# Performance work log

Measured on AMD Instinct MI355X. Metric: run time of the kernel, lower is better.

The kernel has to match this reference:

```python
import jax, jax.numpy as jnp
import numpy as np

B, N, D, H, C = 4, 8192, 1024, 16, 128
HD = D // H  # 64
THRESHOLD = 0.99


def setup_inputs() -> dict:
    key = jax.random.key(0)
    ks = jax.random.split(key, 6)
    std = 0.02
    return {
        "x": jax.random.normal(ks[0], (B, N, D), jnp.float32),
        "Wq": jax.random.normal(ks[1], (D, D), jnp.float32) * std,
        "Wk": jax.random.normal(ks[2], (D, D), jnp.float32) * std,
        "Wv": jax.random.normal(ks[3], (D, D), jnp.float32) * std,
        "Wo": jax.random.normal(ks[4], (D, D), jnp.float32) * std,
        "Wf": jax.random.normal(ks[5], (H, D), jnp.float32) * std,
        "delta": jnp.full((H,), float(np.log(THRESHOLD / (1.0 - THRESHOLD))), jnp.float32),
        "norm_weight": jnp.ones((D,), jnp.float32),
    }


def _chunk_scan(qc, kc, vc, lf):
    # qc,kc,vc: [nc, b, H, C, HD]; lf: [nc, b, H, C] inclusive cumsum of log decay within chunk
    mask = jnp.tril(jnp.ones((C, C), bool))
    def step(S, inputs):
        qb, kb, vb, lb = inputs  # [b,H,C,HD], [b,H,C]
        # inter-chunk: q_i decayed by prod of gates up to i, applied to carried state
        o_inter = jnp.einsum('bhid,bhde->bhie', qb * jnp.exp(lb)[..., None], S)
        # intra-chunk: A_ij = (q_i . k_j) * exp(l_i - l_j), j <= i
        A = jnp.einsum('bhid,bhjd->bhij', qb, kb)
        diff = jnp.where(mask, lb[..., :, None] - lb[..., None, :], -jnp.inf)
        A = A * jnp.exp(diff)
        o_intra = jnp.einsum('bhij,bhjd->bhid', A, vb)
        # state update: S <- exp(l_C) * S + sum_j exp(l_C - l_j) k_j v_j^T
        tot = lb[..., -1]  # [b,H]
        kd = kb * jnp.exp(tot[..., None, None] - lb[..., None])
        S_new = jnp.exp(tot)[..., None, None] * S + jnp.einsum('bhjd,bhje->bhde', kd, vb)
        return S_new, o_inter + o_intra
    S0 = jnp.zeros((qc.shape[1], H, HD, HD), qc.dtype)
    _, o = jax.lax.scan(step, S0, (qc, kc, vc, lf))
    return o  # [nc, b, H, C, HD]


def reference(x, Wq, Wk, Wv, Wo, Wf, delta, norm_weight):
    b, n, d = x.shape
    q = jax.nn.silu(x @ Wq.T)
    k = jax.nn.silu(x @ Wk.T)
    v = x @ Wv.T
    log_f = jax.nn.log_sigmoid(x @ Wf.T + delta)  # [b, n, H] per-head scalar log forget gate
    nc = n // C
    def to_chunks(t):
        return t.reshape(b, nc, C, H, HD).transpose(1, 0, 3, 2, 4)  # [nc,b,H,C,HD]
    qc, kc, vc = map(to_chunks, (q, k, v))
    lf = jnp.cumsum(log_f.reshape(b, nc, C, H).transpose(1, 0, 3, 2), axis=-1)  # [nc,b,H,C]
    o = _chunk_scan(qc, kc, vc, lf)
    o = o.transpose(1, 0, 3, 2, 4).reshape(b, n, d)
    # RMSNorm
    o = o * jax.lax.rsqrt(jnp.mean(o * o, axis=-1, keepdims=True) + 1e-6) * norm_weight
    return o @ Wo.T
```

## Files before the change

kernel.cpp:

```cpp
#include <hip/hip_runtime.h>

typedef unsigned short u16;
typedef __attribute__((ext_vector_type(8))) short bf16x8;
typedef __attribute__((ext_vector_type(4))) short bf16x4;
typedef __attribute__((ext_vector_type(4))) float f32x4;

#define MFMA16(a,b,c) __builtin_amdgcn_mfma_f32_16x16x32_bf16(a,b,c,0,0,0)

__device__ __forceinline__ float bf2f(short s){
  return __uint_as_float(((unsigned)(u16)s) << 16);
}
__device__ __forceinline__ short f2bf(float f){
  unsigned u = __float_as_uint(f);
  return (short)((u + 0x7FFFu + ((u >> 16) & 1u)) >> 16);
}
__device__ __forceinline__ void gload16(const void* g, void* l){
  __builtin_amdgcn_global_load_lds((const __attribute__((address_space(1))) unsigned int*)g,
                                   (__attribute__((address_space(3))) unsigned int*)l, 16, 0, 0);
}
__device__ __forceinline__ float silu_f(float v){ return v / (1.f + __expf(-v)); }

__global__ __launch_bounds__(256) void cvt_kernel(const float* __restrict__ s, u16* __restrict__ d){
  size_t i = ((size_t)blockIdx.x*256 + threadIdx.x)*8;
  float4 a = *(const float4*)(s+i);
  float4 b = *(const float4*)(s+i+4);
  bf16x8 o;
  o[0]=f2bf(a.x); o[1]=f2bf(a.y); o[2]=f2bf(a.z); o[3]=f2bf(a.w);
  o[4]=f2bf(b.x); o[5]=f2bf(b.y); o[6]=f2bf(b.z); o[7]=f2bf(b.w);
  *(bf16x8*)(d+i) = o;
}

template<int MODE>
__global__ __launch_bounds__(256) void gemm_bt(
    const u16* __restrict__ A, const u16* __restrict__ Bw,
    u16* __restrict__ qo, u16* __restrict__ kTo, u16* __restrict__ vTo,
    float* __restrict__ outf)
{
  __shared__ __align__(16) char smem[65536];
  const int tid = threadIdx.x, l = tid & 63, wv = tid >> 6;
  const int m0 = blockIdx.y << 7, n0 = blockIdx.x << 7;
  const int wr = wv >> 1, wc = wv & 1;
  const int srow = wv*8 + (l>>3);
  const int scol = (l&7)*8;

  f32x4 acc[4][4] = {};

  {
    const u16* Ab = A + (size_t)m0*1024;
    const u16* Bb = Bw + (size_t)n0*1024;
    #pragma unroll
    for (int i=0;i<4;i++){
      gload16(Ab + (size_t)(srow + i*32)*1024 + scol, smem + i*4096 + wv*1024);
      gload16(Bb + (size_t)(srow + i*32)*1024 + scol, smem + 16384 + i*4096 + wv*1024);
    }
  }
  for (int kt=0; kt<16; ++kt){
    __syncthreads();
    if (kt+1 < 16){
      const int k0 = (kt+1)*64;
      const u16* Ab = A + (size_t)m0*1024 + k0;
      const u16* Bb = Bw + (size_t)n0*1024 + k0;
      char* lb = smem + ((kt+1)&1)*32768;
      #pragma unroll
      for (int i=0;i<4;i++){
        gload16(Ab + (size_t)(srow + i*32)*1024 + scol, lb + i*4096 + wv*1024);
        gload16(Bb + (size_t)(srow + i*32)*1024 + scol, lb + 16384 + i*4096 + wv*1024);
      }
    }
    const char* la  = smem + (kt&1)*32768;
    const char* lbB = la + 16384;
    #pragma unroll
    for (int ks=0; ks<2; ++ks){
      const int kb = ks*64 + ((l>>4)<<4);
      bf16x8 af[4], bfr[4];
      #pragma unroll
      for (int t=0;t<4;t++){
        af[t]  = *(const bf16x8*)(la  + (wr*64 + t*16 + (l&15))*128 + kb);
        bfr[t] = *(const bf16x8*)(lbB + (wc*64 + t*16 + (l&15))*128 + kb);
      }
      #pragma unroll
      for (int i=0;i<4;i++)
        #pragma unroll
        for (int j=0;j<4;j++)
          acc[i][j] = MFMA16(af[i], bfr[j], acc[i][j]);
    }
  }
  if constexpr (MODE == 1){
    #pragma unroll
    for (int i=0;i<4;i++){
      const int tok = m0 + wr*64 + i*16 + ((l>>4)<<2);
      #pragma unroll
      for (int j=0;j<4;j++){
        const int ch = n0 + wc*64 + j*16 + (l&15);
        #pragma unroll
        for (int r=0;r<4;r++)
          outf[(size_t)(tok+r)*1024 + ch] = acc[i][j][r];
      }
    }
  } else {
    const int nblk = blockIdx.x;
    if (nblk < 8){
      #pragma unroll
      for (int i=0;i<4;i++){
        const int tok = m0 + wr*64 + i*16 + ((l>>4)<<2);
        #pragma unroll
        for (int j=0;j<4;j++){
          const int ch = (nblk<<7) + wc*64 + j*16 + (l&15);
          #pragma unroll
          for (int r=0;r<4;r++)
            qo[(size_t)(tok+r)*1024 + ch] = (u16)f2bf(silu_f(acc[i][j][r]));
        }
      }
    } else {
      const bool dos = nblk < 16;
      u16* T = dos ? kTo : vTo;
      const int cb = (nblk - (dos?8:16))<<7;
      #pragma unroll
      for (int i=0;i<4;i++){
        const int tok0 = m0 + wr*64 + i*16 + ((l>>4)<<2);
        #pragma unroll
        for (int j=0;j<4;j++){
          const int ch = cb + wc*64 + j*16 + (l&15);
          bf16x4 pk;
          #pragma unroll
          for (int r=0;r<4;r++){
            float v = acc[i][j][r];
            if (dos) v = silu_f(v);
            pk[r] = f2bf(v);
          }
          *(bf16x4*)(T + (size_t)ch*32768 + tok0) = pk;
        }
      }
    }
  }
}

__global__ __launch_bounds__(256) void logf_kernel(
  const u16* __restrict__ xbf, const u16* __restrict__ wf,
  const float* __restrict__ delta, float* __restrict__ lfo)
{
  const int tid = threadIdx.x, l = tid&63, wv = tid>>6;
  const int arow = blockIdx.x*64 + wv*16 + (l&15);
  const u16* xr  = xbf + (size_t)arow*1024 + ((l>>4)<<3);
  const u16* wr_ = wf  + (size_t)(l&15)*1024 + ((l>>4)<<3);
  f32x4 acc = {0.f,0.f,0.f,0.f};
  #pragma unroll 4
  for (int kk=0; kk<32; ++kk){
    bf16x8 a = *(const bf16x8*)(xr  + kk*32);
    bf16x8 b = *(const bf16x8*)(wr_ + kk*32);
    acc = MFMA16(a,b,acc);
  }
  const int h = l&15;
  const float dl = delta[h];
  const int trow = blockIdx.x*64 + wv*16 + ((l>>4)<<2);
  #pragma unroll
  for (int r=0;r<4;r++){
    float z = acc[r] + dl;
    lfo[(size_t)(trow + r)*16 + h] = fminf(z, 0.f) - log1pf(__expf(-fabsf(z)));
  }
}

#define P2_SK  16384
#define P2_SKT 32768
#define P2_SVT 49152
__global__ __launch_bounds__(256) void intra_kernel(
  u16* __restrict__ q,
  const u16* __restrict__ kT, const u16* __restrict__ vT,
  const float* __restrict__ lfin, float* __restrict__ tots,
  u16* __restrict__ O, float* __restrict__ BT)
{
  __shared__ __align__(16) char smem[67072];
  float* s_lf = (float*)(smem + 65536);
  float* s_e  = (float*)(smem + 66048);
  float* s_en = (float*)(smem + 66560);
  const int c = blockIdx.x, bh = blockIdx.y;
  const int b = bh >> 4, h = bh & 15;
  const int tid = threadIdx.x, l = tid&63, wv = tid>>6;
  const size_t tok0 = (size_t)b*8192 + (size_t)c*128;

  if (tid < 128) s_lf[tid] = lfin[(tok0 + tid)*16 + h];
  __syncthreads();
  #pragma unroll
  for (int off=1; off<128; off<<=1){
    float v = 0.f;
    if (tid < 128) v = s_lf[tid] + ((tid >= off) ? s_lf[tid-off] : 0.f);
    __syncthreads();
    if (tid < 128) s_lf[tid] = v;
    __syncthreads();
  }
  if (tid < 128){ const float lv = s_lf[tid]; s_e[tid] = __expf(lv); s_en[tid] = __expf(-lv); }
  if (tid == 0) tots[((size_t)b*16 + h)*64 + c] = s_lf[127];
  __syncthreads();

  {
    u16* qb = q + tok0*1024 + h*64;
    #pragma unroll
    for (int it=0; it<4; ++it){
      const int cid = it*256 + tid;
      const int j = cid >> 3, d0 = (cid&7)*8;
      bf16x8 v = *(const bf16x8*)(qb + (size_t)j*1024 + d0);
      *(bf16x8*)(smem + j*128 + ((d0*2) ^ ((j&7)<<4))) = v;
      const float ej = s_e[j];
      bf16x8 o;
      #pragma unroll
      for (int u=0;u<8;u++) o[u] = f2bf(bf2f(v[u]) * ej);
      *(bf16x8*)(qb + (size_t)j*1024 + d0) = o;
    }
    const u16* kb_ = kT + (size_t)(h*64)*32768 + tok0;
    const u16* vb_ = vT + (size_t)(h*64)*32768 + tok0;
    #pragma unroll
    for (int it=0; it<4; ++it){
      const int cid = it*256 + tid;
      const int d = cid >> 4, j0 = (cid&15)*8;
      bf16x8 kv = *(const bf16x8*)(kb_ + (size_t)d*32768 + j0);
      bf16x8 vv = *(const bf16x8*)(vb_ + (size_t)d*32768 + j0);
      bf16x8 ks;
      #pragma unroll
      for (int u=0;u<8;u++) ks[u] = f2bf(bf2f(kv[u]) * s_en[j0+u]);
      *(bf16x8*)(smem + P2_SKT + d*256 + ((j0*2) ^ ((d&15)<<4))) = ks;
      *(bf16x8*)(smem + P2_SVT + d*256 + ((j0*2) ^ ((d&15)<<4))) = vv;
    }
  }
  __syncthreads();

  #pragma unroll
  for (int nn=0; nn<2; ++nn){
    const int nt = wv*2 + nn;
    const int kk = nt >> 1;
    const int ustar = ((nt&1)<<4) + (l&15) - ((l>>4)<<3);
    bf16x8 ib;
    #pragma unroll
    for (int u=0;u<8;u++) ib[u] = (u == ustar) ? (short)0x3F80 : (short)0;
    const int jb = (kk*32 + ((l>>4)<<3))*2;
    #pragma unroll
    for (int mt=0; mt<4; ++mt){
      const int d = mt*16 + (l&15);
      bf16x8 af = *(const bf16x8*)(smem + P2_SKT + d*256 + (jb ^ ((d&15)<<4)));
      f32x4 dd = {0.f,0.f,0.f,0.f};
      dd = MFMA16(af, ib, dd);
      const int jj = nt*16 + (l&15);
      const int d0 = mt*16 + ((l>>4)<<2);
      bf16x4 pk;
      #pragma unroll
      for (int r=0;r<4;r++) pk[r] = f2bf(dd[r]);
      *(bf16x4*)(smem + P2_SK + jj*128 + ((d0*2) ^ ((jj&7)<<4))) = pk;
    }
  }
  __syncthreads();

  f32x4 acc1[2][8] = {};
  const int jt0 = wv, jt1 = 7 - wv;
  #pragma unroll
  for (int ks=0; ks<2; ++ks){
    const int kb = (ks*32 + ((l>>4)<<3))*2;
    bf16x8 aq[8];
    #pragma unroll
    for (int nt=0;nt<8;nt++){
      const int i = nt*16 + (l&15);
      aq[nt] = *(const bf16x8*)(smem + i*128 + (kb ^ ((i&7)<<4)));
    }
    const int jr0 = jt0*16 + (l&15), jr1 = jt1*16 + (l&15);
    bf16x8 ak0 = *(const bf16x8*)(smem + P2_SK + jr0*128 + (kb ^ ((jr0&7)<<4)));
    bf16x8 ak1 = *(const bf16x8*)(smem + P2_SK + jr1*128 + (kb ^ ((jr1&7)<<4)));
    #pragma unroll
    for (int nt=0;nt<8;nt++){
      if (nt >= jt0) acc1[0][nt] = MFMA16(ak0, aq[nt], acc1[0][nt]);
      if (nt >= jt1) acc1[1][nt] = MFMA16(ak1, aq[nt], acc1[1][nt]);
    }
  }
  __syncthreads();

  #pragma unroll
  for (int jj=0;jj<2;jj++){
    const int jt = (jj==0)? jt0 : jt1;
    const int j0 = jt*16 + ((l>>4)<<2);
    #pragma unroll
    for (int nt=0;nt<8;nt++){
      const int i = nt*16 + (l&15);
      bf16x4 pk;
      if (nt < jt){
        #pragma unroll
        for (int r=0;r<4;r++) pk[r] = (short)0;
      } else {
        const float ei = s_e[i];
        #pragma unroll
        for (int r=0;r<4;r++){
          float v = acc1[jj][nt][r] * ei;
          if (nt == jt && (j0 + r) > i) v = 0.f;
          pk[r] = f2bf(v);
        }
      }
      *(bf16x4*)(smem + i*256 + ((j0*2) ^ ((i&15)<<4))) = pk;
    }
  }
  __syncthreads();

  {
    const int nt0 = wv, nt1 = 7 - wv;
    f32x4 oacc[2][4] = {};
    f32x4 bcacc[4] = {};
    #pragma unroll
    for (int kk=0; kk<4; ++kk){
      const int jb = (kk*32 + ((l>>4)<<3))*2;
      bf16x8 av[4];
      #pragma unroll
      for (int mt=0;mt<4;mt++){
        const int e = mt*16 + (l&15);
        av[mt] = *(const bf16x8*)(smem + P2_SVT + e*256 + (jb ^ ((e&15)<<4)));
      }
      const int dr = wv*16 + (l&15);
      bf16x8 akt = *(const bf16x8*)(smem + P2_SKT + dr*256 + (jb ^ ((dr&15)<<4)));
      #pragma unroll
      for (int mt=0;mt<4;mt++) bcacc[mt] = MFMA16(akt, av[mt], bcacc[mt]);
      const int i0 = nt0*16 + (l&15);
      if (kk <= (nt0>>1)){
        bf16x8 ba = *(const bf16x8*)(smem + i0*256 + (jb ^ ((i0&15)<<4)));
        #pragma unroll
        for (int mt=0;mt<4;mt++) oacc[0][mt] = MFMA16(av[mt], ba, oacc[0][mt]);
      }
      const int i1 = nt1*16 + (l&15);
      if (kk <= (nt1>>1)){
        bf16x8 ba = *(const bf16x8*)(smem + i1*256 + (jb ^ ((i1&15)<<4)));
        #pragma unroll
        for (int mt=0;mt<4;mt++) oacc[1][mt] = MFMA16(av[mt], ba, oacc[1][mt]);
      }
    }
    #pragma unroll
    for (int jj=0;jj<2;jj++){
      const int nt = (jj==0)?nt0:nt1;
      const int i = nt*16 + (l&15);
      u16* orow = O + (tok0 + i)*1024 + h*64;
      #pragma unroll
      for (int mt=0;mt<4;mt++){
        const int e0 = mt*16 + ((l>>4)<<2);
        bf16x4 pk;
        #pragma unroll
        for (int r=0;r<4;r++) pk[r] = f2bf(oacc[jj][mt][r]);
        *(bf16x4*)(orow + e0) = pk;
      }
    }
    __syncthreads();
    #pragma unroll
    for (int nt2=0; nt2<4; ++nt2){
      const int e = nt2*16 + (l&15);
      const int d0 = wv*16 + ((l>>4)<<2);
      *(f32x4*)(smem + P2_SKT + e*256 + ((d0*4) ^ ((e&15)<<4))) = bcacc[nt2];
    }
    __syncthreads();
    float* BTo = BT + (((size_t)c*4 + b)*16 + h)*4096;
    #pragma unroll
    for (int u=0;u<4;u++){
      const int fb = tid*64 + u*16;
      const int e = fb >> 8, wi = fb & 255;
      f32x4 vvv = *(const f32x4*)(smem + P2_SKT + e*256 + (wi ^ ((e&15)<<4)));
      *(f32x4*)((char*)BTo + fb) = vvv;
    }
  }
}

__global__ __launch_bounds__(256) void scan_kernel(
  const float* __restrict__ BT, const float* __restrict__ tots, u16* __restrict__ ST)
{
  const int blk = blockIdx.x;
  const int bh = blk >> 2, qt = blk & 3;
  const int tid = threadIdx.x;
  __shared__ float s_tot[64];
  if (tid < 64) s_tot[tid] = tots[(size_t)bh*64 + tid];
  __syncthreads();
  const int flat = qt*1024 + tid*4;
  const float* bp = BT + (size_t)bh*4096 + flat;
  u16* sp = ST + (size_t)bh*4096 + flat;
  const size_t cs = 262144;
  f32x4 S = {0.f,0.f,0.f,0.f};
  f32x4 cur = *(const f32x4*)bp;
  f32x4 nxt = *(const f32x4*)(bp + cs);
  for (int cc=0; cc<64; ++cc){
    bf16x4 pk;
    #pragma unroll
    for (int r=0;r<4;r++) pk[r] = f2bf(S[r]);
    *(bf16x4*)(sp + (size_t)cc*cs) = pk;
    const float et = __expf(s_tot[cc]);
    #pragma unroll
    for (int r=0;r<4;r++) S[r] = et*(S[r] + cur[r]);
    cur = nxt;
    if (cc + 2 < 64) nxt = *(const f32x4*)(bp + (size_t)(cc+2)*cs);
  }
}

__global__ __launch_bounds__(256) void inter_kernel(
  const u16* __restrict__ qg, const u16* __restrict__ ST, u16* __restrict__ O)
{
  __shared__ __align__(16) char smem[24576];
  const int c = blockIdx.x, bh = blockIdx.y;
  const int b = bh>>4, h = bh&15;
  const int tid = threadIdx.x, l = tid&63, wv = tid>>6;
  const size_t tok0 = (size_t)b*8192 + (size_t)c*128;
  const u16* qb = qg + tok0*1024 + h*64;
  #pragma unroll
  for (int it=0; it<4; ++it){
    const int cid = it*256 + tid, j = cid>>3, d0 = (cid&7)*8;
    bf16x8 v = *(const bf16x8*)(qb + (size_t)j*1024 + d0);
    *(bf16x8*)(smem + j*128 + ((d0*2) ^ ((j&7)<<4))) = v;
  }
  const u16* stb = ST + (((size_t)c*4 + b)*16 + h)*4096;
  #pragma unroll
  for (int it=0; it<2; ++it){
    const int cid = it*256 + tid, e = cid>>3, d0 = (cid&7)*8;
    bf16x8 v = *(const bf16x8*)(stb + (size_t)e*64 + d0);
    *(bf16x8*)(smem + 16384 + e*128 + ((d0*2) ^ ((e&7)<<4))) = v;
  }
  __syncthreads();
  f32x4 acc[8] = {};
  #pragma unroll
  for (int ks=0; ks<2; ++ks){
    const int kb = (ks*32 + ((l>>4)<<3))*2;
    const int er = wv*16 + (l&15);
    bf16x8 as = *(const bf16x8*)(smem + 16384 + er*128 + (kb ^ ((er&7)<<4)));
    #pragma unroll
    for (int nt=0;nt<8;nt++){
      const int ir = nt*16 + (l&15);
      bf16x8 bq = *(const bf16x8*)(smem + ir*128 + (kb ^ ((ir&7)<<4)));
      acc[nt] = MFMA16(as, bq, acc[nt]);
    }
  }
  const int e0 = wv*16 + ((l>>4)<<2);
  #pragma unroll
  for (int nt=0;nt<8;nt++){
    const int i = nt*16 + (l&15);
    u16* op = O + (tok0 + i)*1024 + h*64 + e0;
    bf16x4 cu = *(const bf16x4*)op;
    bf16x4 pk;
    #pragma unroll
    for (int r=0;r<4;r++) pk[r] = f2bf(bf2f(cu[r]) + acc[nt][r]);
    *(bf16x4*)op = pk;
  }
}

__global__ __launch_bounds__(256) void rmsnorm_kernel(
  const u16* __restrict__ O, const float* __restrict__ nw, u16* __restrict__ ON)
{
  const int tid = threadIdx.x, l = tid&63, wv = tid>>6;
  const size_t tok = (size_t)blockIdx.x*4 + wv;
  const u16* row = O + tok*1024;
  bf16x8 v0 = *(const bf16x8*)(row + l*8);
  bf16x8 v1 = *(const bf16x8*)(row + 512 + l*8);
  float f0[8], f1[8];
  float ss = 0.f;
  #pragma unroll
  for (int u=0;u<8;u++){ f0[u]=bf2f(v0[u]); f1[u]=bf2f(v1[u]); ss += f0[u]*f0[u] + f1[u]*f1[u]; }
  #pragma unroll
  for (int off=32; off>0; off>>=1) ss += __shfl_xor(ss, off, 64);
  const float rs = rsqrtf(ss*(1.f/1024.f) + 1e-6f);
  bf16x8 o0, o1;
  #pragma unroll
  for (int u=0;u<8;u++){
    o0[u] = f2bf(f0[u]*rs*nw[l*8+u]);
    o1[u] = f2bf(f1[u]*rs*nw[512+l*8+u]);
  }
  *(bf16x8*)(ON + tok*1024 + l*8) = o0;
  *(bf16x8*)(ON + tok*1024 + 512 + l*8) = o1;
}

extern "C" void kernel_launch(void* const* d_in, const int* in_sizes, int n_in,
                              void* d_out, int out_size, void* d_ws, size_t ws_size,
                              hipStream_t stream)
{
  (void)in_sizes; (void)n_in; (void)out_size;
  const float* x  = (const float*)d_in[0];
  const float* Wq = (const float*)d_in[1];
  const float* Wk = (const float*)d_in[2];
  const float* Wv = (const float*)d_in[3];
  const float* Wo = (const float*)d_in[4];
  const float* Wf = (const float*)d_in[5];
  const float* de = (const float*)d_in[6];
  const float* nw = (const float*)d_in[7];
  float* out = (float*)d_out;
  char* ws = (char*)d_ws;
  if (ws_size < 379633664u) return;

  u16*   XBF  = (u16*)(ws + 0);
  u16*   WQKV = (u16*)(ws + 67108864);
  u16*   WOBF = (u16*)(ws + 73400320);
  u16*   WFBF = (u16*)(ws + 75497472);
  u16*   QBUF = (u16*)(ws + 75530240);
  u16*   KTB  = (u16*)(ws + 142639104);
  u16*   VTB  = (u16*)(ws + 209747968);
  u16*   OBUF = (u16*)(ws + 276856832);
  float* LOGF = (float*)(ws + 343965696);
  float* TOTS = (float*)(ws + 346062848);
  u16*   STB  = (u16*)(ws + 346079232);
  float* BTF  = (float*)XBF;

  cvt_kernel<<<16384, 256, 0, stream>>>(x, XBF);
  cvt_kernel<<<512, 256, 0, stream>>>(Wq, WQKV);
  cvt_kernel<<<512, 256, 0, stream>>>(Wk, WQKV + 1048576);
  cvt_kernel<<<512, 256, 0, stream>>>(Wv, WQKV + 2097152);
  cvt_kernel<<<512, 256, 0, stream>>>(Wo, WOBF);
  cvt_kernel<<<8, 256, 0, stream>>>(Wf, WFBF);

  gemm_bt<0><<<dim3(24, 256), 256, 0, stream>>>(XBF, WQKV, QBUF, KTB, VTB, nullptr);
  logf_kernel<<<512, 256, 0, stream>>>(XBF, WFBF, de, LOGF);
  intra_kernel<<<dim3(64, 64), 256, 0, stream>>>(QBUF, KTB, VTB, LOGF, TOTS, OBUF, BTF);
  scan_kernel<<<256, 256, 0, stream>>>(BTF, TOTS, STB);
  inter_kernel<<<dim3(64, 64), 256, 0, stream>>>(QBUF, STB, OBUF);
  rmsnorm_kernel<<<8192, 256, 0, stream>>>(OBUF, nw, QBUF);
  gemm_bt<1><<<dim3(8, 256), 256, 0, stream>>>(QBUF, WOBF, nullptr, nullptr, nullptr, out);
}
```

Before: 890.6 us.

## Replace 128x128 GEMM with 256x256-tile 8-wave GEMM with swizzled LDS

```diff
diff --git a/kernel.cpp b/kernel.cpp
--- a/kernel.cpp
+++ b/kernel.cpp
@@ -19,6 +19,10 @@
                                    (__attribute__((address_space(3))) unsigned int*)l, 16, 0, 0);
 }
 __device__ __forceinline__ float silu_f(float v){ return v / (1.f + __expf(-v)); }
+
+#define FENCE asm volatile("" ::: "memory")
+#define BAR   do{ FENCE; __builtin_amdgcn_s_barrier(); FENCE; }while(0)
+#define LGKM0 do{ asm volatile("s_waitcnt lgkmcnt(0)" ::: "memory"); __builtin_amdgcn_sched_barrier(0); }while(0)
 
 __global__ __launch_bounds__(256) void cvt_kernel(const float* __restrict__ s, u16* __restrict__ d){
   size_t i = ((size_t)blockIdx.x*256 + threadIdx.x)*8;
@@ -31,100 +35,177 @@
 }
 
 template<int MODE>
-__global__ __launch_bounds__(256) void gemm_bt(
+__global__ __launch_bounds__(512) void gemm256(
     const u16* __restrict__ A, const u16* __restrict__ Bw,
     u16* __restrict__ qo, u16* __restrict__ kTo, u16* __restrict__ vTo,
     float* __restrict__ outf)
 {
-  __shared__ __align__(16) char smem[65536];
+  __shared__ __align__(16) char smem[131072];
   const int tid = threadIdx.x, l = tid & 63, wv = tid >> 6;
-  const int m0 = blockIdx.y << 7, n0 = blockIdx.x << 7;
-  const int wr = wv >> 1, wc = wv & 1;
-  const int srow = wv*8 + (l>>3);
-  const int scol = (l&7)*8;
-
-  f32x4 acc[4][4] = {};
-
-  {
-    const u16* Ab = A + (size_t)m0*1024;
-    const u16* Bb = Bw + (size_t)n0*1024;
-    #pragma unroll
-    for (int i=0;i<4;i++){
-      gload16(Ab + (size_t)(srow + i*32)*1024 + scol, smem + i*4096 + wv*1024);
-      gload16(Bb + (size_t)(srow + i*32)*1024 + scol, smem + 16384 + i*4096 + wv*1024);
-    }
-  }
-  for (int kt=0; kt<16; ++kt){
-    __syncthreads();
-    if (kt+1 < 16){
-      const int k0 = (kt+1)*64;
-      const u16* Ab = A + (size_t)m0*1024 + k0;
-      const u16* Bb = Bw + (size_t)n0*1024 + k0;
-      char* lb = smem + ((kt+1)&1)*32768;
-      #pragma unroll
-      for (int i=0;i<4;i++){
-        gload16(Ab + (size_t)(srow + i*32)*1024 + scol, lb + i*4096 + wv*1024);
-        gload16(Bb + (size_t)(srow + i*32)*1024 + scol, lb + 16384 + i*4096 + wv*1024);
-      }
-    }
-    const char* la  = smem + (kt&1)*32768;
-    const char* lbB = la + 16384;
-    #pragma unroll
-    for (int ks=0; ks<2; ++ks){
-      const int kb = ks*64 + ((l>>4)<<4);
-      bf16x8 af[4], bfr[4];
-      #pragma unroll
-      for (int t=0;t<4;t++){
-        af[t]  = *(const bf16x8*)(la  + (wr*64 + t*16 + (l&15))*128 + kb);
-        bfr[t] = *(const bf16x8*)(lbB + (wc*64 + t*16 + (l&15))*128 + kb);
-      }
-      #pragma unroll
-      for (int i=0;i<4;i++)
-        #pragma unroll
-        for (int j=0;j<4;j++)
-          acc[i][j] = MFMA16(af[i], bfr[j], acc[i][j]);
-    }
-  }
+  const int wr = wv >> 2, wc = wv & 3;
+  const int m0 = blockIdx.y << 8, n0 = blockIdx.x << 8;
+  const int sr = (wv << 3) + (l >> 3);
+  const int sc = l & 7;
+  const int lk = l >> 4, ln = l & 15;
+
+  f32x4 acc[8][4] = {};
+
+  auto stA = [&](int u, int h){
+    const u16* src = A + (size_t)(m0 + h*128)*1024 + u*64;
+    char* dst = smem + (u&1)*32768 + h*16384 + wv*1024;
+    #pragma unroll
+    for (int i=0;i<2;i++){
+      const int r = i*64 + sr;
+      gload16(src + (size_t)r*1024 + ((sc ^ (r&7))<<3), dst + i*8192);
+    }
+  };
+  auto stB = [&](int u, int h){
+    const u16* src = Bw + (size_t)(n0 + h*128)*1024 + u*64;
+    char* dst = smem + 65536 + (u&1)*32768 + h*16384 + wv*1024;
+    #pragma unroll
+    for (int i=0;i<2;i++){
+      const int r = i*64 + sr;
+      gload16(src + (size_t)r*1024 + ((sc ^ (r&7))<<3), dst + i*8192);
+    }
+  };
+  auto ldA = [&](int bsel, int row, int ks)->bf16x8 {
+    const int c16 = ((ks<<2) + lk) ^ (row & 7);
+    return *(const bf16x8*)(smem + bsel + row*128 + (c16<<4));
+  };
+  auto ldB = [&](int bsel, int row, int ks)->bf16x8 {
+    const int c16 = ((ks<<2) + lk) ^ (row & 7);
+    return *(const bf16x8*)(smem + 65536 + bsel + row*128 + (c16<<4));
+  };
+
+  stA(0,0); stA(0,1); stB(0,0); stB(0,1); stB(1,0); stB(1,1);
+  asm volatile("s_waitcnt vmcnt(4)" ::: "memory");
+  BAR;
+
+  bf16x8 brg[4][2];
+  #pragma unroll 1
+  for (int u=0; u<16; ++u){
+    const int bsel = (u&1)*32768;
+    {
+      #pragma unroll
+      for (int n=0;n<4;n++){
+        brg[n][0] = ldB(bsel, wc*64 + n*16 + ln, 0);
+        brg[n][1] = ldB(bsel, wc*64 + n*16 + ln, 1);
+      }
+      bf16x8 a00 = ldA(bsel, wr*128 +  0 + ln, 0);
+      bf16x8 a01 = ldA(bsel, wr*128 +  0 + ln, 1);
+      bf16x8 a10 = ldA(bsel, wr*128 + 16 + ln, 0);
+      bf16x8 a11 = ldA(bsel, wr*128 + 16 + ln, 1);
+      if (u+1 < 16) stA(u+1, 0);
+      BAR; LGKM0;
+      __builtin_amdgcn_s_setprio(1);
+      #pragma unroll
+      for (int n=0;n<4;n++){
+        acc[0][n] = MFMA16(a00, brg[n][0], acc[0][n]);
+        acc[0][n] = MFMA16(a01, brg[n][1], acc[0][n]);
+        acc[1][n] = MFMA16(a10, brg[n][0], acc[1][n]);
+        acc[1][n] = MFMA16(a11, brg[n][1], acc[1][n]);
+      }
+      __builtin_amdgcn_s_setprio(0);
+      BAR;
+    }
+    {
+      bf16x8 a00 = ldA(bsel, wr*128 + 32 + ln, 0);
+      bf16x8 a01 = ldA(bsel, wr*128 + 32 + ln, 1);
+      bf16x8 a10 = ldA(bsel, wr*128 + 48 + ln, 0);
+      bf16x8 a11 = ldA(bsel, wr*128 + 48 + ln, 1);
+      if (u+1 < 16) stA(u+1, 1);
+      BAR; LGKM0;
+      __builtin_amdgcn_s_setprio(1);
+      #pragma unroll
+      for (int n=0;n<4;n++){
+        acc[2][n] = MFMA16(a00, brg[n][0], acc[2][n]);
+        acc[2][n] = MFMA16(a01, brg[n][1], acc[2][n]);
+        acc[3][n] = MFMA16(a10, brg[n][0], acc[3][n]);
+        acc[3][n] = MFMA16(a11, brg[n][1], acc[3][n]);
+      }
+      __builtin_amdgcn_s_setprio(0);
+      BAR;
+    }
+    {
+      bf16x8 a00 = ldA(bsel, wr*128 + 64 + ln, 0);
+      bf16x8 a01 = ldA(bsel, wr*128 + 64 + ln, 1);
+      bf16x8 a10 = ldA(bsel, wr*128 + 80 + ln, 0);
+      bf16x8 a11 = ldA(bsel, wr*128 + 80 + ln, 1);
+      if (u+2 < 16) stB(u+2, 0);
+      BAR; LGKM0;
+      __builtin_amdgcn_s_setprio(1);
+      #pragma unroll
+      for (int n=0;n<4;n++){
+        acc[4][n] = MFMA16(a00, brg[n][0], acc[4][n]);
+        acc[4][n] = MFMA16(a01, brg[n][1], acc[4][n]);
+        acc[5][n] = MFMA16(a10, brg[n][0], acc[5][n]);
+        acc[5][n] = MFMA16(a11, brg[n][1], acc[5][n]);
+      }
+      __builtin_amdgcn_s_setprio(0);
+      BAR;
+    }
+    {
+      bf16x8 a00 = ldA(bsel, wr*128 +  96 + ln, 0);
+      bf16x8 a01 = ldA(bsel, wr*128 +  96 + ln, 1);
+      bf16x8 a10 = ldA(bsel, wr*128 + 112 + ln, 0);
+      bf16x8 a11 = ldA(bsel, wr*128 + 112 + ln, 1);
+      if (u+2 < 16) stB(u+2, 1);
+      if (u <= 13)      { asm volatile("s_waitcnt vmcnt(4)" ::: "memory"); }
+      else if (u == 14) { asm volatile("s_waitcnt vmcnt(0)" ::: "memory"); }
+      BAR; LGKM0;
+      __builtin_amdgcn_s_setprio(1);
+      #pragma unroll
+      for (int n=0;n<4;n++){
+        acc[6][n] = MFMA16(a00, brg[n][0], acc[6][n]);
+        acc[6][n] = MFMA16(a01, brg[n][1], acc[6][n]);
+        acc[7][n] = MFMA16(a10, brg[n][0], acc[7][n]);
+        acc[7][n] = MFMA16(a11, brg[n][1], acc[7][n]);
+      }
+      __builtin_amdgcn_s_setprio(0);
+      BAR;
+    }
+  }
+
   if constexpr (MODE == 1){
     #pragma unroll
-    for (int i=0;i<4;i++){
-      const int tok = m0 + wr*64 + i*16 + ((l>>4)<<2);
-      #pragma unroll
-      for (int j=0;j<4;j++){
-        const int ch = n0 + wc*64 + j*16 + (l&15);
+    for (int m=0;m<8;m++){
+      const int tok = m0 + wr*128 + m*16 + lk*4;
+      #pragma unroll
+      for (int n=0;n<4;n++){
+        const int ch = n0 + wc*64 + n*16 + ln;
         #pragma unroll
         for (int r=0;r<4;r++)
-          outf[(size_t)(tok+r)*1024 + ch] = acc[i][j][r];
+          outf[(size_t)(tok+r)*1024 + ch] = acc[m][n][r];
       }
     }
   } else {
     const int nblk = blockIdx.x;
-    if (nblk < 8){
-      #pragma unroll
-      for (int i=0;i<4;i++){
-        const int tok = m0 + wr*64 + i*16 + ((l>>4)<<2);
-        #pragma unroll
-        for (int j=0;j<4;j++){
-          const int ch = (nblk<<7) + wc*64 + j*16 + (l&15);
+    if (nblk < 4){
+      #pragma unroll
+      for (int m=0;m<8;m++){
+        const int tok = m0 + wr*128 + m*16 + lk*4;
+        #pragma unroll
+        for (int n=0;n<4;n++){
+          const int ch = nblk*256 + wc*64 + n*16 + ln;
           #pragma unroll
           for (int r=0;r<4;r++)
-            qo[(size_t)(tok+r)*1024 + ch] = (u16)f2bf(silu_f(acc[i][j][r]));
+            qo[(size_t)(tok+r)*1024 + ch] = (u16)f2bf(silu_f(acc[m][n][r]));
         }
       }
     } else {
-      const bool dos = nblk < 16;
+      const bool dos = nblk < 8;
       u16* T = dos ? kTo : vTo;
-      const int cb = (nblk - (dos?8:16))<<7;
-      #pragma unroll
-      for (int i=0;i<4;i++){
-        const int tok0 = m0 + wr*64 + i*16 + ((l>>4)<<2);
-        #pragma unroll
-        for (int j=0;j<4;j++){
-          const int ch = cb + wc*64 + j*16 + (l&15);
+      const int cb = (nblk & 3) << 8;
+      #pragma unroll
+      for (int m=0;m<8;m++){
+        const int tok0 = m0 + wr*128 + m*16 + lk*4;
+        #pragma unroll
+        for (int n=0;n<4;n++){
+          const int ch = cb + wc*64 + n*16 + ln;
           bf16x4 pk;
           #pragma unroll
           for (int r=0;r<4;r++){
-            float v = acc[i][j][r];
+            float v = acc[m][n][r];
             if (dos) v = silu_f(v);
             pk[r] = f2bf(v);
           }
@@ -498,11 +579,11 @@
   cvt_kernel<<<512, 256, 0, stream>>>(Wo, WOBF);
   cvt_kernel<<<8, 256, 0, stream>>>(Wf, WFBF);
 
-  gemm_bt<0><<<dim3(24, 256), 256, 0, stream>>>(XBF, WQKV, QBUF, KTB, VTB, nullptr);
+  gemm256<0><<<dim3(12, 128), 512, 0, stream>>>(XBF, WQKV, QBUF, KTB, VTB, nullptr);
   logf_kernel<<<512, 256, 0, stream>>>(XBF, WFBF, de, LOGF);
   intra_kernel<<<dim3(64, 64), 256, 0, stream>>>(QBUF, KTB, VTB, LOGF, TOTS, OBUF, BTF);
   scan_kernel<<<256, 256, 0, stream>>>(BTF, TOTS, STB);
   inter_kernel<<<dim3(64, 64), 256, 0, stream>>>(QBUF, STB, OBUF);
   rmsnorm_kernel<<<8192, 256, 0, stream>>>(OBUF, nw, QBUF);
-  gemm_bt<1><<<dim3(8, 256), 256, 0, stream>>>(QBUF, WOBF, nullptr, nullptr, nullptr, out);
-}
+  gemm256<1><<<dim3(4, 128), 512, 0, stream>>>(QBUF, WOBF, nullptr, nullptr, nullptr, out);
+}
```

Result: faster. 796.0 us (-10.6%).
